# Optimization experiments

Hardware: AMD Instinct MI355X
Metric: run time of the kernel (lower is better)

The kernel has to match this reference:

```python
import jax, jax.numpy as jnp
import numpy as np

EPS = 1e-8
TOP_K = 3  # hardcoded in the original forward (torch.topk(sims, 3))


def setup_inputs() -> dict:
    key = jax.random.key(0)
    ks = jax.random.split(key, 6)
    n1, d1 = 4096, 1024
    n2, d2 = 4096, 4096
    V = jax.random.normal(ks[0], (n1, d1), dtype=jnp.float32)
    X = jax.random.normal(ks[1], (n2, d2), dtype=jnp.float32)
    # nn.Linear(visual_dim, text_dim): weight [d2, d1], bias [d2]
    Wv = jax.random.normal(ks[2], (d2, d1), dtype=jnp.float32) * (1.0 / np.sqrt(d1))
    bv = jax.random.normal(ks[3], (d2,), dtype=jnp.float32) * 0.01
    # nn.Linear(top_k, 1): weight [1, 3], bias [1]
    Wf = jax.random.normal(ks[4], (1, TOP_K), dtype=jnp.float32) * (1.0 / np.sqrt(TOP_K))
    bf = jax.random.normal(ks[5], (1,), dtype=jnp.float32) * 0.01
    return {"V": V, "X": X, "Wv": Wv, "bv": bv, "Wf": Wf, "bf": bf}


def reference(V, X, Wv, bv, Wf, bf):
    # project visual tokens into text space: [n1, d2]
    V_proj = V @ Wv.T + bv
    # cosine similarity: normalize queries (full-vector norm) and keys (row norm)
    Qn = X / (jnp.linalg.norm(X, axis=1, keepdims=True) + EPS)          # [n2, d2]
    Kn = V_proj / (jnp.linalg.norm(V_proj, axis=1, keepdims=True) + EPS)  # [n1, d2]
    sims = Qn @ Kn.T                                                     # [n2, n1]
    # per-text-token top-k visual tokens
    _, topk_idx = jax.lax.top_k(sims, TOP_K)                             # [n2, k]
    gathered = V_proj[topk_idx]                                          # [n2, k, d2]
    # fuse over k: Linear(k -> 1) applied along the top-k axis, squeeze -> [n2, d2]
    V_aligned = jnp.einsum('nkd,k->nd', gathered, Wf[0]) + bf[0]
    return jnp.concatenate([V_aligned, X], axis=0)                       # [2*n2, d2]
```

## Files before the change

kernel.cpp:

```cpp
#include <hip/hip_runtime.h>
#include <hip/hip_bf16.h>

constexpr int N1 = 4096;
constexpr int D1 = 1024;
constexpr int N2 = 4096;
constexpr int D2 = 4096;

#define FNEG  (-3.402823466e+38f)
#define IDX_INF 0x7FFFFFFF
#define NCHUNK 32
#define CPR (NCHUNK * 6)
#define FCAP 512
#define CERT_TH 1.5e-3f

using s16x8 = __attribute__((ext_vector_type(8))) short;
using f32x4 = __attribute__((ext_vector_type(4))) float;

static __device__ __forceinline__ unsigned short f2bf(float x) {
    unsigned int u = __float_as_uint(x);
    unsigned int r = (u + 0x7FFFu + ((u >> 16) & 1u)) >> 16;
    return (unsigned short)r;
}
static __device__ __forceinline__ float bf2f(unsigned short v) {
    return __uint_as_float((unsigned)v << 16);
}
static __device__ __forceinline__ void splitbf(float x, unsigned short& h,
                                               unsigned short& l) {
    unsigned short hh = f2bf(x);
    float r = x - __uint_as_float((unsigned)hh << 16);
    h = hh; l = f2bf(r);
}
static __device__ __forceinline__ int swz(int row, int g) {
    return row * 32 + ((g ^ (row & 3)) << 3);
}

static __device__ __forceinline__ void stageF32(const float* src, int ld,
    int rowbase, int k0, unsigned short* H, unsigned short* L, int tid)
{
    const int r = tid >> 1, half = tid & 1;
    const float* p = src + (size_t)(rowbase + r) * ld + k0 + half * 16;
#pragma unroll
    for (int gg = 0; gg < 2; ++gg) {
        const int g = half * 2 + gg;
        float4 v0 = *(const float4*)(p + gg * 8);
        float4 v1 = *(const float4*)(p + gg * 8 + 4);
        float xs[8] = {v0.x, v0.y, v0.z, v0.w, v1.x, v1.y, v1.z, v1.w};
        s16x8 hv, lv;
#pragma unroll
        for (int e = 0; e < 8; ++e) {
            unsigned short h, l; splitbf(xs[e], h, l);
            hv[e] = (short)h; lv[e] = (short)l;
        }
        const int a = swz(r, g);
        *(s16x8*)&H[a] = hv;
        *(s16x8*)&L[a] = lv;
    }
}

static __device__ __forceinline__ void gl_lds16(const void* g, void* l)
{
    __builtin_amdgcn_global_load_lds(
        (const __attribute__((address_space(1))) void*)g,
        (__attribute__((address_space(3))) void*)l, 16, 0, 0);
}

static __device__ __forceinline__ void stageSplitGL(const unsigned short* Hs,
    const unsigned short* Ls, int ld, int rowbase, int k0,
    unsigned short* H, unsigned short* L, int lane, int w)
{
#pragma unroll
    for (int t = 0; t < 2; ++t) {
        const int chunk = w * 128 + t * 64 + lane;
        const int row = chunk >> 2;
        const int gp  = chunk & 3;
        const int g   = gp ^ (row & 3);
        const unsigned short* sh =
            Hs + (size_t)(rowbase + row) * ld + k0 + g * 8;
        const unsigned short* sl =
            Ls + (size_t)(rowbase + row) * ld + k0 + g * 8;
        unsigned short* dh = H + (size_t)(w * 128 + t * 64) * 8;
        unsigned short* dl = L + (size_t)(w * 128 + t * 64) * 8;
        gl_lds16(sh, dh);
        gl_lds16(sl, dl);
    }
}

static __device__ __forceinline__ void stageWvTpre(const unsigned short* Wh,
    const unsigned short* Wl, int k0, int tn,
    unsigned short* H, unsigned short* L, int tid)
{
    const int kk = tid >> 3, cg = tid & 7;
    const int g = kk >> 3, idx = kk & 7;
    const unsigned short* ph = Wh + (size_t)(k0 + kk) * D1 + tn + cg * 16;
    const unsigned short* pl = Wl + (size_t)(k0 + kk) * D1 + tn + cg * 16;
#pragma unroll
    for (int q = 0; q < 4; ++q) {
        ushort4 vh = *(const ushort4*)(ph + q * 4);
        ushort4 vl = *(const ushort4*)(pl + q * 4);
        unsigned short hs[4] = {vh.x, vh.y, vh.z, vh.w};
        unsigned short ls[4] = {vl.x, vl.y, vl.z, vl.w};
#pragma unroll
        for (int e = 0; e < 4; ++e) {
            const int cc = cg * 16 + q * 4 + e;
            const int a = cc * 32 + ((g ^ (cc & 3)) << 3) + idx;
            H[a] = hs[e]; L[a] = ls[e];
        }
    }
}

static __device__ __forceinline__ s16x8 fragRead(const unsigned short* B,
                                                 int rowbase, int lane)
{
    const int row = rowbase + (lane & 15);
    const int g = lane >> 4;
    return *(const s16x8*)&B[row * 32 + ((g ^ (row & 3)) << 3)];
}

#define MFMA3(ACC, AH, AL, BH, BL)                                          \
    ACC = __builtin_amdgcn_mfma_f32_16x16x32_bf16(AH, BH, ACC, 0, 0, 0);    \
    ACC = __builtin_amdgcn_mfma_f32_16x16x32_bf16(AH, BL, ACC, 0, 0, 0);    \
    ACC = __builtin_amdgcn_mfma_f32_16x16x32_bf16(AL, BH, ACC, 0, 0, 0);

static __device__ __forceinline__ void top6f(float v, int i, float* vv, int* ii)
{
#pragma unroll
    for (int s = 0; s < 6; ++s) {
        if (v > vv[s]) {
#pragma unroll
            for (int t = 5; t > s; --t) { vv[t] = vv[t-1]; ii[t] = ii[t-1]; }
            vv[s] = v; ii[s] = i;
            break;
        }
    }
}

__global__ __launch_bounds__(256)
void kDetect(const float* c1, const float* c2, int* flags, int* flagCnt)
{
    __shared__ float red[256];
    float d = 0.f;
    for (int i = threadIdx.x; i < 4096; i += 256) {
        float a = c1[i], b = c2[i];
        d += a * a - b * b;
    }
    red[threadIdx.x] = d;
    __syncthreads();
    for (int st = 128; st > 0; st >>= 1) {
        if (threadIdx.x < st) red[threadIdx.x] += red[threadIdx.x + st];
        __syncthreads();
    }
    if (threadIdx.x == 0) {
        flags[0] = (red[0] < 0.f) ? 1 : 0;
        flagCnt[0] = 0;
    }
}

__global__ __launch_bounds__(256)
void kSplit(const float* src, unsigned short* h, unsigned short* l, int n4)
{
    int i = blockIdx.x * 256 + threadIdx.x;
    if (i >= n4) return;
    float4 v = *(const float4*)(src + (size_t)i * 4);
    float xs[4] = {v.x, v.y, v.z, v.w};
    ushort4 hv, lv;
    unsigned short hh, ll;
    splitbf(xs[0], hh, ll); hv.x = hh; lv.x = ll;
    splitbf(xs[1], hh, ll); hv.y = hh; lv.y = ll;
    splitbf(xs[2], hh, ll); hv.z = hh; lv.z = ll;
    splitbf(xs[3], hh, ll); hv.w = hh; lv.w = ll;
    *(ushort4*)(h + (size_t)i * 4) = hv;
    *(ushort4*)(l + (size_t)i * 4) = lv;
}

__global__ __launch_bounds__(256)
void kSvec(const float* X, const float* bv, float* sXF)
{
    __shared__ double red[256];
    const int row = blockIdx.x;
    double s = 0.0;
    for (int n = threadIdx.x; n < D2; n += 256)
        s += (double)X[(size_t)row * D2 + n] * (double)bv[n];
    red[threadIdx.x] = s;
    __syncthreads();
    for (int st = 128; st > 0; st >>= 1) {
        if (threadIdx.x < st) red[threadIdx.x] += red[threadIdx.x + st];
        __syncthreads();
    }
    if (threadIdx.x == 0) sXF[row] = (float)red[0];
}

__global__ __launch_bounds__(256)
void kNormMfma(const unsigned short* c1h, const unsigned short* c1l,
               const unsigned short* c2h, const unsigned short* c2l,
               const float* bv, const int* flags, float* partial,
               unsigned short* Vph)
{
    const unsigned short* Vh  = flags[0] ? c2h : c1h;
    const unsigned short* Vl  = flags[0] ? c2l : c1l;
    const unsigned short* Wvh = flags[0] ? c1h : c2h;
    const unsigned short* Wvl = flags[0] ? c1l : c2l;
    __shared__ __align__(16) char pool[65536];
    __shared__ float partH[128][2];
    const int tid = threadIdx.x;
    const int lane = tid & 63, w = tid >> 6;
    const int wr = w >> 1, wc = w & 1;
    const int tm = blockIdx.y * 128;
    const int tn = blockIdx.x * 128;

    f32x4 acc[4][4];
#pragma unroll
    for (int i = 0; i < 4; ++i)
#pragma unroll
        for (int j = 0; j < 4; ++j) acc[i][j] = (f32x4){0.f, 0.f, 0.f, 0.f};

    {
        unsigned short* B0 = (unsigned short*)pool;
        stageSplitGL(Vh,  Vl,  D1, tm, 0, B0,        B0 + 4096,  lane, w);
        stageSplitGL(Wvh, Wvl, D1, tn, 0, B0 + 8192, B0 + 12288, lane, w);
    }
    __syncthreads();

    for (int k0 = 0; k0 < D1; k0 += 32) {
        const int cur = (k0 >> 5) & 1;
        unsigned short* CB = (unsigned short*)(pool + cur * 32768);
        if (k0 + 32 < D1) {
            unsigned short* NB = (unsigned short*)(pool + (cur ^ 1) * 32768);
            stageSplitGL(Vh,  Vl,  D1, tm, k0 + 32, NB,        NB + 4096,
                         lane, w);
            stageSplitGL(Wvh, Wvl, D1, tn, k0 + 32, NB + 8192, NB + 12288,
                         lane, w);
        }
        s16x8 ah[4], al[4], bh[4], bl[4];
#pragma unroll
        for (int f = 0; f < 4; ++f) {
            ah[f] = fragRead(CB,         wr * 64 + f * 16, lane);
            al[f] = fragRead(CB + 4096,  wr * 64 + f * 16, lane);
            bh[f] = fragRead(CB + 8192,  wc * 64 + f * 16, lane);
            bl[f] = fragRead(CB + 12288, wc * 64 + f * 16, lane);
        }
#pragma unroll
        for (int fm = 0; fm < 4; ++fm)
#pragma unroll
            for (int fn = 0; fn < 4; ++fn) {
                MFMA3(acc[fm][fn], ah[fm], al[fm], bh[fn], bl[fn]);
            }
        __syncthreads();
    }

    float bvv[4];
#pragma unroll
    for (int fn = 0; fn < 4; ++fn)
        bvv[fn] = bv[tn + wc * 64 + fn * 16 + (lane & 15)];
#pragma unroll
    for (int fm = 0; fm < 4; ++fm)
#pragma unroll
        for (int r = 0; r < 4; ++r) {
            const int lrow = wr * 64 + fm * 16 + (lane >> 4) * 4 + r;
            float rs = 0.f;
#pragma unroll
            for (int fn = 0; fn < 4; ++fn) {
                float v = acc[fm][fn][r] + bvv[fn];
                Vph[(size_t)(tm + lrow) * D2 +
                    (tn + wc * 64 + fn * 16 + (lane & 15))] = f2bf(v);
                rs += v * v;
            }
            rs += __shfl_xor(rs, 1, 64);
            rs += __shfl_xor(rs, 2, 64);
            rs += __shfl_xor(rs, 4, 64);
            rs += __shfl_xor(rs, 8, 64);
            if ((lane & 15) == 0) partH[lrow][wc] = rs;
        }
    __syncthreads();
    if (tid < 128)
        partial[(size_t)(tm + tid) * 32 + blockIdx.x] =
            partH[tid][0] + partH[tid][1];
}

__global__ __launch_bounds__(256)
void kInv(const float* partial, float* invnF)
{
    int j = blockIdx.x * 256 + threadIdx.x;
    float s = 0.f;
    for (int cb = 0; cb < 32; ++cb) s += partial[(size_t)j * 32 + cb];
    invnF[j] = 1.f / (sqrtf(s) + 1e-8f);
}

__global__ __launch_bounds__(256)
void mfmaZ(const float* X,
           const unsigned short* c1h, const unsigned short* c1l,
           const unsigned short* c2h, const unsigned short* c2l,
           const int* flags, unsigned short* Zh, unsigned short* Zl)
{
    const unsigned short* Wvh = flags[0] ? c1h : c2h;
    const unsigned short* Wvl = flags[0] ? c1l : c2l;
    __shared__ unsigned short AH[4096], AL[4096], BH[4096], BL[4096];
    const int tid = threadIdx.x;
    const int lane = tid & 63, w = tid >> 6;
    const int wr = w >> 1, wc = w & 1;
    const int tm = blockIdx.y * 128;
    const int tn = blockIdx.x * 128;

    f32x4 acc[4][4];
#pragma unroll
    for (int i = 0; i < 4; ++i)
#pragma unroll
        for (int j = 0; j < 4; ++j) acc[i][j] = (f32x4){0.f, 0.f, 0.f, 0.f};

    for (int k0 = 0; k0 < D2; k0 += 32) {
        stageF32(X, D2, tm, k0, AH, AL, tid);
        stageWvTpre(Wvh, Wvl, k0, tn, BH, BL, tid);
        __syncthreads();
        s16x8 ah[4], al[4], bh[4], bl[4];
#pragma unroll
        for (int f = 0; f < 4; ++f) {
            ah[f] = fragRead(AH, wr * 64 + f * 16, lane);
            al[f] = fragRead(AL, wr * 64 + f * 16, lane);
            bh[f] = fragRead(BH, wc * 64 + f * 16, lane);
            bl[f] = fragRead(BL, wc * 64 + f * 16, lane);
        }
#pragma unroll
        for (int fm = 0; fm < 4; ++fm)
#pragma unroll
            for (int fn = 0; fn < 4; ++fn) {
                MFMA3(acc[fm][fn], ah[fm], al[fm], bh[fn], bl[fn]);
            }
        __syncthreads();
    }
#pragma unroll
    for (int fm = 0; fm < 4; ++fm)
#pragma unroll
        for (int fn = 0; fn < 4; ++fn)
#pragma unroll
            for (int r = 0; r < 4; ++r) {
                int row = tm + wr * 64 + fm * 16 + (lane >> 4) * 4 + r;
                int col = tn + wc * 64 + fn * 16 + (lane & 15);
                unsigned short h, l;
                splitbf(acc[fm][fn][r], h, l);
                size_t o = (size_t)row * D1 + col;
                Zh[o] = h; Zl[o] = l;
            }
}

__global__ __launch_bounds__(256)
void mfmaS(const unsigned short* Zh, const unsigned short* Zl,
           const unsigned short* c1h, const unsigned short* c1l,
           const unsigned short* c2h, const unsigned short* c2l,
           const float* invnF, const float* sXF, const int* flags,
           float* candV, int* candI)
{
    const unsigned short* Vh = flags[0] ? c2h : c1h;
    const unsigned short* Vl = flags[0] ? c2l : c1l;
    __shared__ __align__(16) char pool[65536];
    float* Ct   = (float*)pool;
    float* pv   = (float*)(pool + 33792);
    int*   pi   = (int*)  (pool + 36864);
    float* invs = (float*)(pool + 39936);

    const int tid = threadIdx.x;
    const int lane = tid & 63, w = tid >> 6;
    const int wr = w >> 1, wc = w & 1;
    const int tm = blockIdx.y * 128;
    const int tn = blockIdx.x * 128;

    f32x4 acc[4][4];
#pragma unroll
    for (int i = 0; i < 4; ++i)
#pragma unroll
        for (int j = 0; j < 4; ++j) acc[i][j] = (f32x4){0.f, 0.f, 0.f, 0.f};

    {
        unsigned short* B0 = (unsigned short*)pool;
        stageSplitGL(Zh, Zl, D1, tm, 0, B0,        B0 + 4096,  lane, w);
        stageSplitGL(Vh, Vl, D1, tn, 0, B0 + 8192, B0 + 12288, lane, w);
    }
    __syncthreads();

    for (int k0 = 0; k0 < D1; k0 += 32) {
        const int cur = (k0 >> 5) & 1;
        unsigned short* CB = (unsigned short*)(pool + cur * 32768);
        if (k0 + 32 < D1) {
            unsigned short* NB = (unsigned short*)(pool + (cur ^ 1) * 32768);
            stageSplitGL(Zh, Zl, D1, tm, k0 + 32, NB,        NB + 4096,
                         lane, w);
            stageSplitGL(Vh, Vl, D1, tn, k0 + 32, NB + 8192, NB + 12288,
                         lane, w);
        }
        s16x8 ah[4], al[4], bh[4], bl[4];
#pragma unroll
        for (int f = 0; f < 4; ++f) {
            ah[f] = fragRead(CB,         wr * 64 + f * 16, lane);
            al[f] = fragRead(CB + 4096,  wr * 64 + f * 16, lane);
            bh[f] = fragRead(CB + 8192,  wc * 64 + f * 16, lane);
            bl[f] = fragRead(CB + 12288, wc * 64 + f * 16, lane);
        }
#pragma unroll
        for (int fm = 0; fm < 4; ++fm)
#pragma unroll
            for (int fn = 0; fn < 4; ++fn) {
                MFMA3(acc[fm][fn], ah[fm], al[fm], bh[fn], bl[fn]);
            }
        __syncthreads();
    }

    if (tid < 128) invs[tid] = invnF[tn + tid];
    for (int h = 0; h < 2; ++h) {
        __syncthreads();
        if (wr == h) {
#pragma unroll
            for (int fm = 0; fm < 4; ++fm)
#pragma unroll
                for (int fn = 0; fn < 4; ++fn)
#pragma unroll
                    for (int r = 0; r < 4; ++r) {
                        int lr = fm * 16 + (lane >> 4) * 4 + r;
                        int c  = wc * 64 + fn * 16 + (lane & 15);
                        Ct[lr * 132 + c] = acc[fm][fn][r];
                    }
        }
        __syncthreads();
        if (tid < 128) {
            int r = tid >> 1, seg = tid & 1;
            float sxf = sXF[tm + h * 64 + r];
            float vv[6]; int ii[6];
#pragma unroll
            for (int s = 0; s < 6; ++s) { vv[s] = FNEG; ii[s] = IDX_INF; }
            for (int cc = 0; cc < 64; ++cc) {
                int c = seg * 64 + cc;
                float v = (Ct[r * 132 + c] + sxf) * invs[c];
                top6f(v, tn + c, vv, ii);
            }
#pragma unroll
            for (int s = 0; s < 6; ++s) {
                pv[(r * 2 + seg) * 6 + s] = vv[s];
                pi[(r * 2 + seg) * 6 + s] = ii[s];
            }
        }
        __syncthreads();
        if (tid < 64) {
            float vv[6]; int ii[6];
#pragma unroll
            for (int s = 0; s < 6; ++s) { vv[s] = FNEG; ii[s] = IDX_INF; }
            for (int seg = 0; seg < 2; ++seg)
                for (int s = 0; s < 6; ++s)
                    top6f(pv[(tid * 2 + seg) * 6 + s],
                          pi[(tid * 2 + seg) * 6 + s], vv, ii);
            int row = tm + h * 64 + tid;
#pragma unroll
            for (int s = 0; s < 6; ++s) {
                candV[(size_t)row * CPR + blockIdx.x * 6 + s] = vv[s];
                candI[(size_t)row * CPR + blockIdx.x * 6 + s] = ii[s];
            }
        }
    }
}

__global__ __launch_bounds__(64)
void kMergeCert(const float* candV, const int* candI, int* tidx,
                int* flagCnt, int* flagRow, int* flagCand)
{
    if (threadIdx.x != 0) return;
    const int row = blockIdx.x;
    float vv[6]; int ii[6];
    for (int s = 0; s < 6; ++s) { vv[s] = FNEG; ii[s] = IDX_INF; }
    for (int c = 0; c < CPR; ++c)
        top6f(candV[(size_t)row * CPR + c], candI[(size_t)row * CPR + c],
              vv, ii);
    tidx[row * 3 + 0] = ii[0];
    tidx[row * 3 + 1] = ii[1];
    tidx[row * 3 + 2] = ii[2];
    bool cert = (vv[0] - vv[1] > CERT_TH) &&
                (vv[1] - vv[2] > CERT_TH) &&
                (vv[2] - vv[3] > CERT_TH);
    if (!cert) {
        int idx = atomicAdd(flagCnt, 1);
        if (idx < FCAP) {
            flagRow[idx] = row;
            for (int s = 0; s < 6; ++s) flagCand[idx * 6 + s] = ii[s];
        }
    }
}

__global__ __launch_bounds__(256)
void kExactPart(const int* flagCnt, const int* flagRow, const int* flagCand,
                const float* c1, const float* c2, const int* flags,
                const float* X, const float* bv, double* exPart)
{
    const int z = blockIdx.y;
    if (z >= flagCnt[0] || z >= FCAP) return;
    const float* V  = flags[0] ? c2 : c1;
    const float* Wv = flags[0] ? c1 : c2;
    const int row = flagRow[z];
    int js[6];
#pragma unroll
    for (int s = 0; s < 6; ++s) js[s] = flagCand[z * 6 + s];

    double dot[6] = {0,0,0,0,0,0}, nrm[6] = {0,0,0,0,0,0};
    const int nbase = blockIdx.x * 512;
#pragma unroll
    for (int t = 0; t < 2; ++t) {
        const int n = nbase + threadIdx.x * 2 + t;
        double v[6];
        const double bb = (double)bv[n];
#pragma unroll
        for (int s = 0; s < 6; ++s) v[s] = bb;
        const float* wrow = Wv + (size_t)n * D1;
        for (int k = 0; k < D1; ++k) {
            double wv = (double)wrow[k];
#pragma unroll
            for (int s = 0; s < 6; ++s)
                v[s] = fma((double)V[(size_t)js[s] * D1 + k], wv, v[s]);
        }
        const double xn = (double)X[(size_t)row * D2 + n];
#pragma unroll
        for (int s = 0; s < 6; ++s) {
            dot[s] = fma(xn, v[s], dot[s]);
            nrm[s] = fma(v[s], v[s], nrm[s]);
        }
    }
    __shared__ double red[256];
    for (int s = 0; s < 6; ++s) {
        red[threadIdx.x] = dot[s];
        __syncthreads();
        for (int st = 128; st > 0; st >>= 1) {
            if (threadIdx.x < st) red[threadIdx.x] += red[threadIdx.x + st];
            __syncthreads();
        }
        if (threadIdx.x == 0)
            exPart[(((size_t)z * 8 + blockIdx.x) * 6 + s) * 2 + 0] = red[0];
        __syncthreads();
        red[threadIdx.x] = nrm[s];
        __syncthreads();
        for (int st = 128; st > 0; st >>= 1) {
            if (threadIdx.x < st) red[threadIdx.x] += red[threadIdx.x + st];
            __syncthreads();
        }
        if (threadIdx.x == 0)
            exPart[(((size_t)z * 8 + blockIdx.x) * 6 + s) * 2 + 1] = red[0];
        __syncthreads();
    }
}

__global__ __launch_bounds__(64)
void kExactFinal(const int* flagCnt, const int* flagRow, const int* flagCand,
                 const double* exPart, int* tidx)
{
    const int z = blockIdx.x;
    if (z >= flagCnt[0] || z >= FCAP) return;
    if (threadIdx.x != 0) return;
    double sc[6]; int js[6];
    for (int s = 0; s < 6; ++s) {
        double dot = 0.0, nrm = 0.0;
        for (int c = 0; c < 8; ++c) {
            dot += exPart[(((size_t)z * 8 + c) * 6 + s) * 2 + 0];
            nrm += exPart[(((size_t)z * 8 + c) * 6 + s) * 2 + 1];
        }
        sc[s] = dot * (1.0 / (sqrt(nrm) + 1e-8));
        js[s] = flagCand[z * 6 + s];
    }
    int ord[6] = {0,1,2,3,4,5};
    for (int a = 0; a < 5; ++a)
        for (int b = a + 1; b < 6; ++b) {
            bool swp = (sc[ord[b]] > sc[ord[a]]) ||
                       (sc[ord[b]] == sc[ord[a]] && js[ord[b]] < js[ord[a]]);
            if (swp) { int t = ord[a]; ord[a] = ord[b]; ord[b] = t; }
        }
    const int row = flagRow[z];
    tidx[row * 3 + 0] = js[ord[0]];
    tidx[row * 3 + 1] = js[ord[1]];
    tidx[row * 3 + 2] = js[ord[2]];
}

__global__ __launch_bounds__(256)
void kGatherVa(const unsigned short* Vph, const int* tidx,
               const float* Wf, const float* bfp, float* outVa)
{
    const int row = blockIdx.x;
    const int i0 = tidx[row*3+0], i1 = tidx[row*3+1], i2 = tidx[row*3+2];
    const float w0 = Wf[0], w1 = Wf[1], w2 = Wf[2], b = bfp[0];
    const unsigned short* p0 = Vph + (size_t)i0 * D2;
    const unsigned short* p1 = Vph + (size_t)i1 * D2;
    const unsigned short* p2 = Vph + (size_t)i2 * D2;
    float* o = outVa + (size_t)row * D2;
    for (int c = threadIdx.x * 8; c < D2; c += 256 * 8) {
        s16x8 a = *(const s16x8*)(p0 + c);
        s16x8 d = *(const s16x8*)(p1 + c);
        s16x8 e = *(const s16x8*)(p2 + c);
        float out[8];
#pragma unroll
        for (int t = 0; t < 8; ++t)
            out[t] = w0 * bf2f((unsigned short)a[t]) +
                     w1 * bf2f((unsigned short)d[t]) +
                     w2 * bf2f((unsigned short)e[t]) + b;
        *(float4*)(o + c)     = *(float4*)&out[0];
        *(float4*)(o + c + 4) = *(float4*)&out[4];
    }
}

extern "C" void kernel_launch(void* const* d_in, const int* in_sizes, int n_in,
                              void* d_out, int out_size, void* d_ws, size_t ws_size,
                              hipStream_t stream)
{
    const float *c1 = nullptr, *c2 = nullptr, *X = nullptr;
    const float *bv = nullptr, *Wf = nullptr, *bfp = nullptr;
    for (int i = 0; i < n_in; ++i) {
        const float* p = (const float*)d_in[i];
        switch (in_sizes[i]) {
            case 16777216: X = p; break;
            case 4194304:  if (!c1) c1 = p; else c2 = p; break;
            case 4096:     bv = p; break;
            case 3:        Wf = p; break;
            case 1:        bfp = p; break;
            default: break;
        }
    }

    float* out_f = (float*)d_out;
    float* outVa = out_f;
    float* outX  = out_f + (size_t)N2 * D2;

    int* flags   = (int*)d_ws;
    int* flagCnt = (int*)((char*)d_ws + 128);
    char* C0 = (char*)d_ws + 1024;
    float* sXF     = (float*)(C0);
    float* invnF   = (float*)(C0 + 16384);
    int*   tidx    = (int*)  (C0 + 32768);
    float* partial = (float*)(C0 + 98304);
    float* candV   = (float*)(C0 + 622592);
    int*   candI   = (int*)  (C0 + 3768320);
    int*   flagRow = (int*)  (C0 + 6914048);
    int*   flagCand= (int*)  (C0 + 6916096);
    double* exPart = (double*)(C0 + 6928384);
    unsigned short* Zh = (unsigned short*)(C0 + 8388608);
    unsigned short* Zl = (unsigned short*)(C0 + 16777216);

    char* up = (char*)outX;
    unsigned short* c1h = (unsigned short*)(up);
    unsigned short* c1l = (unsigned short*)(up + 8388608);
    unsigned short* c2h = (unsigned short*)(up + 16777216);
    unsigned short* c2l = (unsigned short*)(up + 25165824);
    unsigned short* Vph = (unsigned short*)(up + 33554432);

    kDetect<<<1, 256, 0, stream>>>(c1, c2, flags, flagCnt);
    kSplit<<<4096, 256, 0, stream>>>(c1, c1h, c1l, N1 * D1 / 4);
    kSplit<<<4096, 256, 0, stream>>>(c2, c2h, c2l, N1 * D1 / 4);
    kSvec<<<N2, 256, 0, stream>>>(X, bv, sXF);

    dim3 gN(D2 / 128, N1 / 128);
    kNormMfma<<<gN, 256, 0, stream>>>(c1h, c1l, c2h, c2l, bv, flags,
                                      partial, Vph);
    kInv<<<16, 256, 0, stream>>>(partial, invnF);

    dim3 gZ(D1 / 128, N2 / 128);
    mfmaZ<<<gZ, 256, 0, stream>>>(X, c1h, c1l, c2h, c2l, flags, Zh, Zl);

    dim3 gS(N1 / 128, N2 / 128);
    mfmaS<<<gS, 256, 0, stream>>>(Zh, Zl, c1h, c1l, c2h, c2l,
                                  invnF, sXF, flags, candV, candI);

    kMergeCert<<<N2, 64, 0, stream>>>(candV, candI, tidx,
                                      flagCnt, flagRow, flagCand);
    dim3 gE(8, FCAP);
    kExactPart<<<gE, 256, 0, stream>>>(flagCnt, flagRow, flagCand,
                                       c1, c2, flags, X, bv, exPart);
    kExactFinal<<<FCAP, 64, 0, stream>>>(flagCnt, flagRow, flagCand,
                                         exPart, tidx);

    kGatherVa<<<N2, 256, 0, stream>>>(Vph, tidx, Wf, bfp, outVa);

    hipMemcpyAsync(outX, X, (size_t)N2 * D2 * sizeof(float),
                   hipMemcpyDeviceToDevice, stream);
}
```

Measured before the change: 1.542 ms.

## Rescore flagged rows via projected X·Wv instead of recomputing V_proj rows

The exact fallback for uncertain top-k rows no longer recomputes six full projected key rows in double precision per flagged row. It first computes z = X_row·Wv in double (batched four rows per block, with X held in shared memory). Each candidate is then scored as (z·V_j + X·bv)·invnorm_j, reusing double-precision norms and bias dot products from earlier kernels. This cuts the fallback work enough that the certainty threshold is tightened and the flag capacity raised to 1024. The trade-off is that the candidate norms now come from the approximate split-bf16 projection rather than an exact recompute.

```diff
diff --git a/kernel.cpp b/kernel.cpp
--- a/kernel.cpp
+++ b/kernel.cpp
@@ -10,8 +10,9 @@
 #define IDX_INF 0x7FFFFFFF
 #define NCHUNK 32
 #define CPR (NCHUNK * 6)
-#define FCAP 512
-#define CERT_TH 1.5e-3f
+#define FCAP 1024
+#define ZPB 4
+#define CERT_TH 2.0e-4f
 
 using s16x8 = __attribute__((ext_vector_type(8))) short;
 using f32x4 = __attribute__((ext_vector_type(4))) float;
@@ -173,7 +174,7 @@
 }
 
 __global__ __launch_bounds__(256)
-void kSvec(const float* X, const float* bv, float* sXF)
+void kSvec(const float* X, const float* bv, float* sXF, double* sXD)
 {
     __shared__ double red[256];
     const int row = blockIdx.x;
@@ -186,7 +187,7 @@
         if (threadIdx.x < st) red[threadIdx.x] += red[threadIdx.x + st];
         __syncthreads();
     }
-    if (threadIdx.x == 0) sXF[row] = (float)red[0];
+    if (threadIdx.x == 0) { sXF[row] = (float)red[0]; sXD[row] = red[0]; }
 }
 
 __global__ __launch_bounds__(256)
@@ -277,12 +278,14 @@
 }
 
 __global__ __launch_bounds__(256)
-void kInv(const float* partial, float* invnF)
+void kInv(const float* partial, float* invnF, double* invnD)
 {
     int j = blockIdx.x * 256 + threadIdx.x;
-    float s = 0.f;
-    for (int cb = 0; cb < 32; ++cb) s += partial[(size_t)j * 32 + cb];
-    invnF[j] = 1.f / (sqrtf(s) + 1e-8f);
+    double s = 0.0;
+    for (int cb = 0; cb < 32; ++cb) s += (double)partial[(size_t)j * 32 + cb];
+    double iv = 1.0 / (sqrt(s) + 1e-8);
+    invnD[j] = iv;
+    invnF[j] = (float)iv;
 }
 
 __global__ __launch_bounds__(256)
@@ -480,94 +483,96 @@
     }
 }
 
-__global__ __launch_bounds__(256)
-void kExactPart(const int* flagCnt, const int* flagRow, const int* flagCand,
-                const float* c1, const float* c2, const int* flags,
-                const float* X, const float* bv, double* exPart)
-{
-    const int z = blockIdx.y;
-    if (z >= flagCnt[0] || z >= FCAP) return;
-    const float* V  = flags[0] ? c2 : c1;
+__global__ __launch_bounds__(512)
+void kZx(const int* flagCnt, const int* flagRow,
+         const float* c1, const float* c2, const int* flags,
+         const float* X, double* Zx)
+{
     const float* Wv = flags[0] ? c1 : c2;
-    const int row = flagRow[z];
-    int js[6];
-#pragma unroll
-    for (int s = 0; s < 6; ++s) js[s] = flagCand[z * 6 + s];
-
-    double dot[6] = {0,0,0,0,0,0}, nrm[6] = {0,0,0,0,0,0};
-    const int nbase = blockIdx.x * 512;
-#pragma unroll
-    for (int t = 0; t < 2; ++t) {
-        const int n = nbase + threadIdx.x * 2 + t;
-        double v[6];
-        const double bb = (double)bv[n];
-#pragma unroll
-        for (int s = 0; s < 6; ++s) v[s] = bb;
-        const float* wrow = Wv + (size_t)n * D1;
-        for (int k = 0; k < D1; ++k) {
-            double wv = (double)wrow[k];
-#pragma unroll
-            for (int s = 0; s < 6; ++s)
-                v[s] = fma((double)V[(size_t)js[s] * D1 + k], wv, v[s]);
-        }
-        const double xn = (double)X[(size_t)row * D2 + n];
-#pragma unroll
-        for (int s = 0; s < 6; ++s) {
-            dot[s] = fma(xn, v[s], dot[s]);
-            nrm[s] = fma(v[s], v[s], nrm[s]);
-        }
-    }
-    __shared__ double red[256];
-    for (int s = 0; s < 6; ++s) {
-        red[threadIdx.x] = dot[s];
-        __syncthreads();
-        for (int st = 128; st > 0; st >>= 1) {
-            if (threadIdx.x < st) red[threadIdx.x] += red[threadIdx.x + st];
-            __syncthreads();
-        }
-        if (threadIdx.x == 0)
-            exPart[(((size_t)z * 8 + blockIdx.x) * 6 + s) * 2 + 0] = red[0];
-        __syncthreads();
-        red[threadIdx.x] = nrm[s];
-        __syncthreads();
-        for (int st = 128; st > 0; st >>= 1) {
-            if (threadIdx.x < st) red[threadIdx.x] += red[threadIdx.x + st];
-            __syncthreads();
-        }
-        if (threadIdx.x == 0)
-            exPart[(((size_t)z * 8 + blockIdx.x) * 6 + s) * 2 + 1] = red[0];
-        __syncthreads();
+    const int nact = min(flagCnt[0], FCAP);
+    const int z0 = blockIdx.x * ZPB;
+    if (z0 >= nact) return;
+    const int tid = threadIdx.x;
+    __shared__ float Xs[ZPB][D2];
+    const int na = min(ZPB, nact - z0);
+    for (int zz = 0; zz < na; ++zz) {
+        const float* xr = X + (size_t)flagRow[z0 + zz] * D2;
+        for (int i = tid * 4; i < D2; i += 512 * 4)
+            *(float4*)&Xs[zz][i] = *(const float4*)(xr + i);
+    }
+    for (int zz = na; zz < ZPB; ++zz)
+        for (int i = tid * 4; i < D2; i += 512 * 4)
+            *(float4*)&Xs[zz][i] = (float4){0.f, 0.f, 0.f, 0.f};
+    __syncthreads();
+
+    const int c2i = tid * 2;
+    double acc[ZPB][2];
+#pragma unroll
+    for (int zz = 0; zz < ZPB; ++zz) { acc[zz][0] = 0.0; acc[zz][1] = 0.0; }
+
+#pragma unroll 4
+    for (int n = 0; n < D2; ++n) {
+        float2 wv2 = *(const float2*)(Wv + (size_t)n * D1 + c2i);
+        const double wx = (double)wv2.x, wy = (double)wv2.y;
+#pragma unroll
+        for (int zz = 0; zz < ZPB; ++zz) {
+            const double xv = (double)Xs[zz][n];
+            acc[zz][0] = fma(xv, wx, acc[zz][0]);
+            acc[zz][1] = fma(xv, wy, acc[zz][1]);
+        }
+    }
+    for (int zz = 0; zz < na; ++zz) {
+        Zx[(size_t)(z0 + zz) * D1 + c2i]     = acc[zz][0];
+        Zx[(size_t)(z0 + zz) * D1 + c2i + 1] = acc[zz][1];
     }
 }
 
 __global__ __launch_bounds__(64)
-void kExactFinal(const int* flagCnt, const int* flagRow, const int* flagCand,
-                 const double* exPart, int* tidx)
+void kScore6(const int* flagCnt, const int* flagRow, const int* flagCand,
+             const double* Zx, const float* c1, const float* c2,
+             const int* flags, const double* sXD, const double* invnD,
+             int* tidx)
 {
     const int z = blockIdx.x;
     if (z >= flagCnt[0] || z >= FCAP) return;
-    if (threadIdx.x != 0) return;
+    const float* V = flags[0] ? c2 : c1;
+    const int lane = threadIdx.x;
+
+    double zr[16];
+#pragma unroll
+    for (int t = 0; t < 16; ++t)
+        zr[t] = Zx[(size_t)z * D1 + t * 64 + lane];
+
     double sc[6]; int js[6];
     for (int s = 0; s < 6; ++s) {
-        double dot = 0.0, nrm = 0.0;
-        for (int c = 0; c < 8; ++c) {
-            dot += exPart[(((size_t)z * 8 + c) * 6 + s) * 2 + 0];
-            nrm += exPart[(((size_t)z * 8 + c) * 6 + s) * 2 + 1];
-        }
-        sc[s] = dot * (1.0 / (sqrt(nrm) + 1e-8));
         js[s] = flagCand[z * 6 + s];
-    }
-    int ord[6] = {0,1,2,3,4,5};
-    for (int a = 0; a < 5; ++a)
-        for (int b = a + 1; b < 6; ++b) {
-            bool swp = (sc[ord[b]] > sc[ord[a]]) ||
-                       (sc[ord[b]] == sc[ord[a]] && js[ord[b]] < js[ord[a]]);
-            if (swp) { int t = ord[a]; ord[a] = ord[b]; ord[b] = t; }
-        }
-    const int row = flagRow[z];
-    tidx[row * 3 + 0] = js[ord[0]];
-    tidx[row * 3 + 1] = js[ord[1]];
-    tidx[row * 3 + 2] = js[ord[2]];
+        const float* vr = V + (size_t)js[s] * D1;
+        double d = 0.0;
+#pragma unroll
+        for (int t = 0; t < 16; ++t)
+            d = fma(zr[t], (double)vr[t * 64 + lane], d);
+#pragma unroll
+        for (int off = 1; off < 64; off <<= 1)
+            d += __shfl_xor(d, off, 64);
+        sc[s] = d;
+    }
+    if (lane == 0) {
+        const int row = flagRow[z];
+        const double sx = sXD[row];
+        for (int s = 0; s < 6; ++s)
+            sc[s] = (sc[s] + sx) * invnD[js[s]];
+        int ord[6] = {0, 1, 2, 3, 4, 5};
+        for (int a = 0; a < 5; ++a)
+            for (int b = a + 1; b < 6; ++b) {
+                bool swp = (sc[ord[b]] > sc[ord[a]]) ||
+                           (sc[ord[b]] == sc[ord[a]] &&
+                            js[ord[b]] < js[ord[a]]);
+                if (swp) { int t = ord[a]; ord[a] = ord[b]; ord[b] = t; }
+            }
+        tidx[row * 3 + 0] = js[ord[0]];
+        tidx[row * 3 + 1] = js[ord[1]];
+        tidx[row * 3 + 2] = js[ord[2]];
+    }
 }
 
 __global__ __launch_bounds__(256)
@@ -621,15 +626,16 @@
     int* flags   = (int*)d_ws;
     int* flagCnt = (int*)((char*)d_ws + 128);
     char* C0 = (char*)d_ws + 1024;
-    float* sXF     = (float*)(C0);
-    float* invnF   = (float*)(C0 + 16384);
-    int*   tidx    = (int*)  (C0 + 32768);
-    float* partial = (float*)(C0 + 98304);
-    float* candV   = (float*)(C0 + 622592);
-    int*   candI   = (int*)  (C0 + 3768320);
-    int*   flagRow = (int*)  (C0 + 6914048);
-    int*   flagCand= (int*)  (C0 + 6916096);
-    double* exPart = (double*)(C0 + 6928384);
+    float*  sXF     = (float*) (C0);
+    float*  invnF   = (float*) (C0 + 16384);
+    int*    tidx    = (int*)   (C0 + 32768);
+    double* sXD     = (double*)(C0 + 81920);
+    double* invnD   = (double*)(C0 + 114688);
+    float*  partial = (float*) (C0 + 147456);
+    float*  candV   = (float*) (C0 + 671744);
+    int*    candI   = (int*)   (C0 + 3817472);
+    int*    flagRow = (int*)   (C0 + 6963200);
+    int*    flagCand= (int*)   (C0 + 6967296);
     unsigned short* Zh = (unsigned short*)(C0 + 8388608);
     unsigned short* Zl = (unsigned short*)(C0 + 16777216);
 
@@ -639,16 +645,17 @@
     unsigned short* c2h = (unsigned short*)(up + 16777216);
     unsigned short* c2l = (unsigned short*)(up + 25165824);
     unsigned short* Vph = (unsigned short*)(up + 33554432);
+    double* Zx = (double*)(up);
 
     kDetect<<<1, 256, 0, stream>>>(c1, c2, flags, flagCnt);
     kSplit<<<4096, 256, 0, stream>>>(c1, c1h, c1l, N1 * D1 / 4);
     kSplit<<<4096, 256, 0, stream>>>(c2, c2h, c2l, N1 * D1 / 4);
-    kSvec<<<N2, 256, 0, stream>>>(X, bv, sXF);
+    kSvec<<<N2, 256, 0, stream>>>(X, bv, sXF, sXD);
 
     dim3 gN(D2 / 128, N1 / 128);
     kNormMfma<<<gN, 256, 0, stream>>>(c1h, c1l, c2h, c2l, bv, flags,
                                       partial, Vph);
-    kInv<<<16, 256, 0, stream>>>(partial, invnF);
+    kInv<<<16, 256, 0, stream>>>(partial, invnF, invnD);
 
     dim3 gZ(D1 / 128, N2 / 128);
     mfmaZ<<<gZ, 256, 0, stream>>>(X, c1h, c1l, c2h, c2l, flags, Zh, Zl);
@@ -659,11 +666,11 @@
 
     kMergeCert<<<N2, 64, 0, stream>>>(candV, candI, tidx,
                                       flagCnt, flagRow, flagCand);
-    dim3 gE(8, FCAP);
-    kExactPart<<<gE, 256, 0, stream>>>(flagCnt, flagRow, flagCand,
-                                       c1, c2, flags, X, bv, exPart);
-    kExactFinal<<<FCAP, 64, 0, stream>>>(flagCnt, flagRow, flagCand,
-                                         exPart, tidx);
+
+    kZx<<<FCAP / ZPB, 512, 0, stream>>>(flagCnt, flagRow, c1, c2, flags,
+                                        X, Zx);
+    kScore6<<<FCAP, 64, 0, stream>>>(flagCnt, flagRow, flagCand, Zx,
+                                     c1, c2, flags, sXD, invnD, tidx);
 
     kGatherVa<<<N2, 256, 0, stream>>>(Vph, tidx, Wf, bfp, outVa);
 
```

After: 1.501 ms. 2.7% less time.
